# Performance work log

Hardware: AMD Instinct MI355X
Metric: run time of the kernel (lower is better)

The kernel has to match this reference:

```python
import jax, jax.numpy as jnp
import numpy as np

T, B, I, H = 512, 64, 1024, 1024
SIGMA = 0.01

def setup_inputs() -> dict:
    key = jax.random.key(0)
    k1, k2, k3 = jax.random.split(key, 3)
    X = jax.random.normal(k1, (T, B, I), dtype=jnp.float32)
    W_xh = jax.random.normal(k2, (I, H), dtype=jnp.float32) * SIGMA
    W_hh = jax.random.normal(k3, (H, H), dtype=jnp.float32) * SIGMA
    b_h = jnp.zeros((H,), dtype=jnp.float32)
    return {"X": X, "W_xh": W_xh, "W_hh": W_hh, "b_h": b_h}

def reference(X, W_xh, W_hh, b_h):
    # Precompute input projection for all timesteps in one big GEMM: [T,B,I]@[I,H]
    Xp = jnp.einsum('tbi,ih->tbh', X, W_xh) + b_h
    state0 = jnp.zeros((X.shape[1], W_hh.shape[0]), dtype=X.dtype)

    def step(state, xp_t):
        new_state = jnp.tanh(xp_t + state @ W_hh)
        return new_state, new_state

    final_state, outputs = jax.lax.scan(step, state0, Xp)
    return outputs, final_state
```

## Files before the change

### kernel.cpp

```cpp
#include <hip/hip_runtime.h>
#include <hip/hip_bf16.h>
#include <stdint.h>

typedef short bf16x8 __attribute__((ext_vector_type(8)));
typedef float f32x4  __attribute__((ext_vector_type(4)));
typedef unsigned int u32x4 __attribute__((ext_vector_type(4)));
typedef unsigned int u32x2 __attribute__((ext_vector_type(2)));

static __device__ __forceinline__ unsigned short bf16_rne(float f) {
    unsigned u = __builtin_bit_cast(unsigned, f);
    unsigned r = u + 0x7fffu + ((u >> 16) & 1u);
    return (unsigned short)(r >> 16);
}
static __device__ __forceinline__ float bf16tof(unsigned short h) {
    unsigned u = ((unsigned)h) << 16;
    return __builtin_bit_cast(float, u);
}

__global__ __launch_bounds__(256) void k_transpose(const float* __restrict__ W,
                                                   unsigned short* __restrict__ Wt) {
    __shared__ float tile[64][65];
    int bx = blockIdx.x & 15, by = blockIdx.x >> 4;
    int n0 = bx * 64, k0 = by * 64;
    int tx = threadIdx.x & 63, ty = threadIdx.x >> 6;
#pragma unroll
    for (int p = 0; p < 16; ++p) {
        int r = p * 4 + ty;
        tile[r][tx] = W[(size_t)(k0 + r) * 1024 + n0 + tx];
    }
    __syncthreads();
#pragma unroll
    for (int p = 0; p < 16; ++p) {
        int r = p * 4 + ty;
        Wt[(size_t)(n0 + r) * 1024 + k0 + tx] = bf16_rne(tile[tx][r]);
    }
}

#define LDA 80

__global__ __launch_bounds__(256) void k_xpgemm(const float* __restrict__ X,
                                                const unsigned short* __restrict__ Wt,
                                                const float* __restrict__ bh,
                                                unsigned short* __restrict__ Xp) {
    __shared__ __align__(16) unsigned char ldsA[128 * LDA];
    __shared__ __align__(16) unsigned char ldsB[128 * LDA];
    int p = blockIdx.x;
    int lo = (p & 7) * 256 + (p >> 3);
    int mt = lo >> 3, nt = lo & 7;
    int m0 = mt * 128, n0 = nt * 128;
    int tid = threadIdx.x;
    int lane = tid & 63, wid = tid >> 6;
    int wr = wid >> 1, wc = wid & 1;
    int mw = wr * 64, nw = wc * 64;
    int l15 = lane & 15, kg = lane >> 4;

    f32x4 acc[4][4] = {};
    int arow = tid >> 3, as = tid & 7;
    int brow = tid >> 2, bs = tid & 3;

    for (int kt = 0; kt < 32; ++kt) {
#pragma unroll
        for (int pp = 0; pp < 4; ++pp) {
            int r = pp * 32 + arow;
            const float4 v = *(const float4*)(X + (size_t)(m0 + r) * 1024 + kt * 32 + as * 4);
            unsigned lo32 = ((unsigned)bf16_rne(v.y) << 16) | bf16_rne(v.x);
            unsigned hi32 = ((unsigned)bf16_rne(v.w) << 16) | bf16_rne(v.z);
            *(uint2*)(ldsA + r * LDA + as * 8) = make_uint2(lo32, hi32);
        }
#pragma unroll
        for (int pp = 0; pp < 2; ++pp) {
            int r = pp * 64 + brow;
            uint4 v = *(const uint4*)(Wt + (size_t)(n0 + r) * 1024 + kt * 32 + bs * 8);
            *(uint4*)(ldsB + r * LDA + bs * 16) = v;
        }
        __syncthreads();
        bf16x8 af[4];
#pragma unroll
        for (int i = 0; i < 4; ++i)
            af[i] = *(const bf16x8*)(ldsA + (mw + 16 * i + l15) * LDA + kg * 16);
#pragma unroll
        for (int j = 0; j < 4; ++j) {
            bf16x8 bfj = *(const bf16x8*)(ldsB + (nw + 16 * j + l15) * LDA + kg * 16);
#pragma unroll
            for (int i = 0; i < 4; ++i)
                acc[i][j] = __builtin_amdgcn_mfma_f32_16x16x32_bf16(af[i], bfj, acc[i][j], 0, 0, 0);
        }
        __syncthreads();
    }
#pragma unroll
    for (int j = 0; j < 4; ++j) {
        int col = n0 + nw + 16 * j + l15;
        float bias = bh[col];
#pragma unroll
        for (int i = 0; i < 4; ++i) {
            int rb = m0 + mw + 16 * i + kg * 4;
#pragma unroll
            for (int r = 0; r < 4; ++r)
                Xp[(size_t)(rb + r) * 1024 + col] = bf16_rne(acc[i][j][r] + bias);
        }
    }
}

#define SB0 __builtin_amdgcn_sched_barrier(0)
#define WV0 asm volatile("s_waitcnt vmcnt(0)" ::: "memory")

template<int S> static __device__ __forceinline__ void ld16s(u32x4& d, uint64_t a) {
    if constexpr (S) asm volatile("global_load_dwordx4 %0, %1, off sc0" : "=v"(d) : "v"(a) : "memory");
    else             asm volatile("global_load_dwordx4 %0, %1, off sc1" : "=v"(d) : "v"(a) : "memory");
}
template<int S> static __device__ __forceinline__ void st8s(uint64_t a, u32x2 v) {
    if constexpr (S) asm volatile("global_store_dwordx2 %0, %1, off sc0" :: "v"(a), "v"(v) : "memory");
    else             asm volatile("global_store_dwordx2 %0, %1, off sc1" :: "v"(a), "v"(v) : "memory");
}
template<int S> static __device__ __forceinline__ void stds(uint64_t a, unsigned v) {
    if constexpr (S) asm volatile("global_store_dword %0, %1, off sc0" :: "v"(a), "v"(v) : "memory");
    else             asm volatile("global_store_dword %0, %1, off sc1" :: "v"(a), "v"(v) : "memory");
}
template<int S> static __device__ __forceinline__ unsigned lddw_wait(uint64_t a) {
    unsigned f;
    if constexpr (S) asm volatile("global_load_dword %0, %1, off sc0\n\ts_waitcnt vmcnt(0)" : "=v"(f) : "v"(a) : "memory");
    else             asm volatile("global_load_dword %0, %1, off sc1\n\ts_waitcnt vmcnt(0)" : "=v"(f) : "v"(a) : "memory");
    return f;
}
static __device__ __forceinline__ void st_sys(uint64_t a, unsigned v) {
    asm volatile("global_store_dword %0, %1, off sc0 sc1" :: "v"(a), "v"(v) : "memory");
}
static __device__ __forceinline__ unsigned ld_sys_wait(uint64_t a) {
    unsigned f;
    asm volatile("global_load_dword %0, %1, off sc0 sc1\n\ts_waitcnt vmcnt(0)" : "=v"(f) : "v"(a) : "memory");
    return f;
}

template<int S>
static __device__ __forceinline__ void scan_main(
    const float* __restrict__ Whh, const unsigned short* __restrict__ Xp,
    unsigned short* __restrict__ hbuf, unsigned* __restrict__ flags,
    float* __restrict__ out, unsigned char* lds, int chain, int mypos, int tid) {

    const int lane = tid & 63, wid = tid >> 6;
    const int l15 = lane & 15, kg = lane >> 4;
    const int jt = mypos * 128 + wid * 16;
    const int b  = chain * 16 + l15;
    const int jl = jt + kg * 4;

    bf16x8 w[32];
#pragma unroll
    for (int i = 0; i < 32; ++i)
#pragma unroll
        for (int e = 0; e < 8; ++e)
            w[i][e] = (short)bf16_rne(Whh[(size_t)(i * 32 + kg * 8 + e) * 1024 + jt + l15]);

    const uint64_t hb_c = (uint64_t)hbuf + (uint64_t)chain * 65536;
    const uint64_t fl_c = (uint64_t)flags + (uint64_t)chain * 64;
    const uint64_t fpoll = fl_c + (uint64_t)wid * 4;
    const uint64_t myflag = fl_c + (uint64_t)mypos * 4;

    const uint64_t crd = hb_c + (uint64_t)(lane >> 2) * 2048 + wid * 256 + (lane & 3) * 64;
    unsigned char* ldsw = lds + (lane >> 2) * 2064 + wid * 256 + (lane & 3) * 64;
    const unsigned char* lrd = lds + l15 * 2064 + kg * 16;

    const uint64_t hwr  = hb_c + (uint64_t)l15 * 2048 + (uint64_t)jl * 2;
    const uint64_t xpb  = (uint64_t)Xp + ((uint64_t)b * 1024 + jl) * 2;
    const uint64_t outb = (uint64_t)out + ((uint64_t)b * 1024 + jl) * 4;

    u32x2 xr;
    asm volatile("global_load_dwordx2 %0, %1, off" : "=v"(xr) : "v"(xpb) : "memory");

    f32x4 hv = {0.f, 0.f, 0.f, 0.f};

    for (int t = 0; t < 512; ++t) {
        if (t > 0) {
            unsigned tt = (unsigned)t;
            for (;;) { unsigned f = lddw_wait<S>(fpoll); if (__all(f >= tt)) break; }
        }
        u32x4 c0, c1, c2, c3;
        const uint64_t ca = crd + (uint64_t)(t & 1) * 32768;
        ld16s<S>(c0, ca); ld16s<S>(c1, ca + 16); ld16s<S>(c2, ca + 32); ld16s<S>(c3, ca + 48);
        WV0; SB0;
        *(u32x4*)(ldsw)      = c0; *(u32x4*)(ldsw + 16) = c1;
        *(u32x4*)(ldsw + 32) = c2; *(u32x4*)(ldsw + 48) = c3;
        __syncthreads();

        f32x4 a0 = {0.f, 0.f, 0.f, 0.f}, a1 = {0.f, 0.f, 0.f, 0.f};
        f32x4 a2 = {0.f, 0.f, 0.f, 0.f}, a3 = {0.f, 0.f, 0.f, 0.f};
#pragma unroll
        for (int ks = 0; ks < 8; ++ks) {
            a0 = __builtin_amdgcn_mfma_f32_16x16x32_bf16(
                w[4 * ks + 0], *(const bf16x8*)(lrd + (4 * ks + 0) * 64), a0, 0, 0, 0);
            a1 = __builtin_amdgcn_mfma_f32_16x16x32_bf16(
                w[4 * ks + 1], *(const bf16x8*)(lrd + (4 * ks + 1) * 64), a1, 0, 0, 0);
            a2 = __builtin_amdgcn_mfma_f32_16x16x32_bf16(
                w[4 * ks + 2], *(const bf16x8*)(lrd + (4 * ks + 2) * 64), a2, 0, 0, 0);
            a3 = __builtin_amdgcn_mfma_f32_16x16x32_bf16(
                w[4 * ks + 3], *(const bf16x8*)(lrd + (4 * ks + 3) * 64), a3, 0, 0, 0);
        }
        f32x4 acc = (a0 + a1) + (a2 + a3);

        float xpf[4] = { bf16tof((unsigned short)(xr[0] & 0xffffu)),
                         bf16tof((unsigned short)(xr[0] >> 16)),
                         bf16tof((unsigned short)(xr[1] & 0xffffu)),
                         bf16tof((unsigned short)(xr[1] >> 16)) };
        unsigned hb16[4];
#pragma unroll
        for (int r = 0; r < 4; ++r) {
            float z = acc[r] + xpf[r];
            z = fminf(fmaxf(z, -15.f), 15.f);
            float e = __expf(2.f * z);
            float v = (e - 1.f) / (e + 1.f);
            hv[r] = v;
            hb16[r] = (unsigned)bf16_rne(v);
        }

        if (t < 511) {
            u32x2 hh = { hb16[0] | (hb16[1] << 16), hb16[2] | (hb16[3] << 16) };
            st8s<S>(hwr + (uint64_t)((t + 1) & 1) * 32768, hh);
            WV0;
        }
        __syncthreads();
        if (t < 511 && tid == 0) stds<S>(myflag, (unsigned)(t + 1));

        if (t < 511)
            asm volatile("global_load_dwordx2 %0, %1, off"
                         : "=v"(xr) : "v"(xpb + (uint64_t)(t + 1) * 131072) : "memory");
        asm volatile("global_store_dwordx4 %0, %1, off"
                     :: "v"(outb + (uint64_t)t * 262144), "v"(hv) : "memory");
    }
    asm volatile("global_store_dwordx4 %0, %1, off"
                 :: "v"((uint64_t)out + ((uint64_t)33554432 + (uint64_t)b * 1024 + jl) * 4),
                    "v"(hv) : "memory");
}

__global__ __launch_bounds__(512) void k_scan(const float* __restrict__ Whh,
                                              const unsigned short* __restrict__ Xp,
                                              unsigned short* __restrict__ hbuf,
                                              unsigned int* flags,
                                              unsigned int* aux,
                                              float* __restrict__ out) {
    __shared__ __align__(16) unsigned char lds[16 * 2064];
    const int wgid = blockIdx.x, tid = threadIdx.x;
    const int lane = tid & 63, wid = tid >> 6;
    const int c8 = wgid & 7;
    if (c8 >= 4) return;
    const int chain = c8, mypos = wgid >> 3;
    const int windex = mypos * 4 + chain;
    const uint64_t A = (uint64_t)aux;
    const uint64_t F = (uint64_t)flags;

    unsigned xcc;
    asm volatile("s_getreg_b32 %0, hwreg(20, 0, 32)" : "=s"(xcc));
    xcc &= 7u;
    if (tid == 0) {
        if (mypos == 0) {
            uint64_t tm;
            asm volatile("s_memtime %0" : "=s"(tm));
            st_sys(F + 960 + (uint64_t)chain * 4, ((unsigned)tm ^ (unsigned)(tm >> 32)) | 1u);
        }
        st_sys(A + (uint64_t)windex * 4, xcc);
        WV0;
        st_sys(A + 128 + (uint64_t)windex * 4, 1u);
    }
    {
        uint64_t p = A + 128 + (uint64_t)(chain + 4 * (lane & 7)) * 4;
        for (;;) { unsigned f = ld_sys_wait(p); if (__all(f == 1u)) break; }
    }
    unsigned mapok;
    {
        unsigned x = ld_sys_wait(A + (uint64_t)(chain + 4 * (lane & 7)) * 4);
        unsigned x0 = (unsigned)__shfl((int)x, 0);
        mapok = __all(x == x0) ? 1u : 0u;
    }
    const unsigned nonce = ld_sys_wait(F + 960 + (uint64_t)chain * 4);

    const int l15 = lane & 15, kg = lane >> 4;
    const uint64_t hwr0 = (uint64_t)hbuf + (uint64_t)chain * 65536 +
                          (uint64_t)l15 * 2048 +
                          (uint64_t)(mypos * 128 + wid * 16 + kg * 4) * 2;
    if (mapok) {
#pragma unroll
        for (int par = 0; par < 2; ++par) {
            stds<1>(hwr0 + (uint64_t)par * 32768, 0u);
            stds<1>(hwr0 + (uint64_t)par * 32768 + 4, 0u);
        }
        if (tid == 0) {
            stds<1>(F + (uint64_t)chain * 64 + (uint64_t)mypos * 4, 0u);
            stds<1>(A + 640 + (uint64_t)windex * 4, 0u);
        }
        WV0;
    }
    __syncthreads();
    if (tid == 0) st_sys(A + 256 + (uint64_t)windex * 4, 1u);
    {
        uint64_t p = A + 256 + (uint64_t)(chain + 4 * (lane & 7)) * 4;
        for (;;) { unsigned f = ld_sys_wait(p); if (__all(f == 1u)) break; }
    }

    unsigned localok = mapok;
    if (mapok) {
        if (tid == 0) stds<1>(A + 640 + (uint64_t)windex * 4, nonce ^ (unsigned)windex);
        uint64_t p = A + 640 + (uint64_t)(chain + 4 * (lane & 7)) * 4;
        unsigned expv = nonce ^ (unsigned)(chain + 4 * (lane & 7));
        int ok = 0;
        for (int it = 0; it < 5000; ++it) {
            unsigned f = lddw_wait<1>(p);
            if (__all(f == expv)) { ok = 1; break; }
        }
        localok = (unsigned)ok;
    }
    if (tid == 0) {
        st_sys(A + 384 + (uint64_t)windex * 4, localok ? 1u : 2u);
        WV0;
        st_sys(A + 512 + (uint64_t)windex * 4, 1u);
    }
    {
        uint64_t p = A + 512 + (uint64_t)(chain + 4 * (lane & 7)) * 4;
        for (;;) { unsigned f = ld_sys_wait(p); if (__all(f == 1u)) break; }
    }
    unsigned v = ld_sys_wait(A + 384 + (uint64_t)(chain + 4 * (lane & 7)) * 4);
    const int FAST = __all(v == 1u) ? 1 : 0;
    __syncthreads();

    if (FAST) scan_main<1>(Whh, Xp, hbuf, flags, out, lds, chain, mypos, tid);
    else      scan_main<0>(Whh, Xp, hbuf, flags, out, lds, chain, mypos, tid);
}

extern "C" void kernel_launch(void* const* d_in, const int* in_sizes, int n_in,
                              void* d_out, int out_size, void* d_ws, size_t ws_size,
                              hipStream_t stream) {
    const float* X   = (const float*)d_in[0];
    const float* Wxh = (const float*)d_in[1];
    const float* Whh = (const float*)d_in[2];
    const float* bh  = (const float*)d_in[3];
    float* out = (float*)d_out;
    unsigned char* ws = (unsigned char*)d_ws;

    unsigned short* Wt    = (unsigned short*)(ws);
    unsigned short* Xp    = (unsigned short*)(ws + 2097152);
    unsigned short* hbuf  = (unsigned short*)(ws + 69206016);
    unsigned int*   flags = (unsigned int*)(ws + 69468160);
    unsigned int*   aux   = (unsigned int*)(ws + 69468416);

    hipMemsetAsync(ws + 69206016, 0, 263168, stream);
    hipLaunchKernelGGL(k_transpose, dim3(256), dim3(256), 0, stream, Wxh, Wt);
    hipLaunchKernelGGL(k_xpgemm, dim3(2048), dim3(256), 0, stream, X, Wt, bh, Xp);
    hipLaunchKernelGGL(k_scan, dim3(64), dim3(512), 0, stream, Whh, Xp, hbuf, flags, aux, out);
}
```

Before: 2.099 ms.

## Add a dedicated I/O wavefront to stage Xp loads and output stores via LDS

Each scan workgroup grows from 8 to 9 waves. The extra wave prefetches the Xp slices two steps ahead into double-buffered LDS and writes the previous step's hidden outputs from LDS to global memory. This takes the per-step Xp load and output store off the latency-critical recurrence waves. The cost is an extra barrier per step, coordinated with a double barrier in the I/O wave, more LDS use, and a larger block.

```diff
diff --git a/kernel.cpp b/kernel.cpp
--- a/kernel.cpp
+++ b/kernel.cpp
@@ -103,6 +103,10 @@
 
 #define SB0 __builtin_amdgcn_sched_barrier(0)
 #define WV0 asm volatile("s_waitcnt vmcnt(0)" ::: "memory")
+#define WLG0 asm volatile("s_waitcnt lgkmcnt(0)" ::: "memory")
+#define BAR do { asm volatile("" ::: "memory"); __builtin_amdgcn_sched_barrier(0); \
+                 __builtin_amdgcn_s_barrier(); \
+                 __builtin_amdgcn_sched_barrier(0); asm volatile("" ::: "memory"); } while (0)
 
 template<int S> static __device__ __forceinline__ void ld16s(u32x4& d, uint64_t a) {
     if constexpr (S) asm volatile("global_load_dwordx4 %0, %1, off sc0" : "=v"(d) : "v"(a) : "memory");
@@ -130,6 +134,12 @@
     asm volatile("global_load_dword %0, %1, off sc0 sc1\n\ts_waitcnt vmcnt(0)" : "=v"(f) : "v"(a) : "memory");
     return f;
 }
+#define LDX8(d, a) asm volatile("global_load_dwordx2 %0, %1, off" : "=v"(d) : "v"(a) : "memory")
+#define STOUT4(a, v) asm volatile("global_store_dwordx4 %0, %1, off" :: "v"(a), "v"(v) : "memory")
+
+#define L_SLICE 0
+#define L_OUT   33024
+#define L_XP    49408
 
 template<int S>
 static __device__ __forceinline__ void scan_main(
@@ -138,105 +148,146 @@
     float* __restrict__ out, unsigned char* lds, int chain, int mypos, int tid) {
 
     const int lane = tid & 63, wid = tid >> 6;
-    const int l15 = lane & 15, kg = lane >> 4;
-    const int jt = mypos * 128 + wid * 16;
-    const int b  = chain * 16 + l15;
-    const int jl = jt + kg * 4;
-
-    bf16x8 w[32];
-#pragma unroll
-    for (int i = 0; i < 32; ++i)
-#pragma unroll
-        for (int e = 0; e < 8; ++e)
-            w[i][e] = (short)bf16_rne(Whh[(size_t)(i * 32 + kg * 8 + e) * 1024 + jt + l15]);
-
     const uint64_t hb_c = (uint64_t)hbuf + (uint64_t)chain * 65536;
     const uint64_t fl_c = (uint64_t)flags + (uint64_t)chain * 64;
-    const uint64_t fpoll = fl_c + (uint64_t)wid * 4;
-    const uint64_t myflag = fl_c + (uint64_t)mypos * 4;
-
-    const uint64_t crd = hb_c + (uint64_t)(lane >> 2) * 2048 + wid * 256 + (lane & 3) * 64;
-    unsigned char* ldsw = lds + (lane >> 2) * 2064 + wid * 256 + (lane & 3) * 64;
-    const unsigned char* lrd = lds + l15 * 2064 + kg * 16;
-
-    const uint64_t hwr  = hb_c + (uint64_t)l15 * 2048 + (uint64_t)jl * 2;
-    const uint64_t xpb  = (uint64_t)Xp + ((uint64_t)b * 1024 + jl) * 2;
-    const uint64_t outb = (uint64_t)out + ((uint64_t)b * 1024 + jl) * 4;
-
-    u32x2 xr;
-    asm volatile("global_load_dwordx2 %0, %1, off" : "=v"(xr) : "v"(xpb) : "memory");
-
-    f32x4 hv = {0.f, 0.f, 0.f, 0.f};
-
-    for (int t = 0; t < 512; ++t) {
-        if (t > 0) {
-            unsigned tt = (unsigned)t;
-            for (;;) { unsigned f = lddw_wait<S>(fpoll); if (__all(f >= tt)) break; }
-        }
-        u32x4 c0, c1, c2, c3;
-        const uint64_t ca = crd + (uint64_t)(t & 1) * 32768;
-        ld16s<S>(c0, ca); ld16s<S>(c1, ca + 16); ld16s<S>(c2, ca + 32); ld16s<S>(c3, ca + 48);
-        WV0; SB0;
-        *(u32x4*)(ldsw)      = c0; *(u32x4*)(ldsw + 16) = c1;
-        *(u32x4*)(ldsw + 32) = c2; *(u32x4*)(ldsw + 48) = c3;
-        __syncthreads();
-
-        f32x4 a0 = {0.f, 0.f, 0.f, 0.f}, a1 = {0.f, 0.f, 0.f, 0.f};
-        f32x4 a2 = {0.f, 0.f, 0.f, 0.f}, a3 = {0.f, 0.f, 0.f, 0.f};
-#pragma unroll
-        for (int ks = 0; ks < 8; ++ks) {
-            a0 = __builtin_amdgcn_mfma_f32_16x16x32_bf16(
-                w[4 * ks + 0], *(const bf16x8*)(lrd + (4 * ks + 0) * 64), a0, 0, 0, 0);
-            a1 = __builtin_amdgcn_mfma_f32_16x16x32_bf16(
-                w[4 * ks + 1], *(const bf16x8*)(lrd + (4 * ks + 1) * 64), a1, 0, 0, 0);
-            a2 = __builtin_amdgcn_mfma_f32_16x16x32_bf16(
-                w[4 * ks + 2], *(const bf16x8*)(lrd + (4 * ks + 2) * 64), a2, 0, 0, 0);
-            a3 = __builtin_amdgcn_mfma_f32_16x16x32_bf16(
-                w[4 * ks + 3], *(const bf16x8*)(lrd + (4 * ks + 3) * 64), a3, 0, 0, 0);
-        }
-        f32x4 acc = (a0 + a1) + (a2 + a3);
-
-        float xpf[4] = { bf16tof((unsigned short)(xr[0] & 0xffffu)),
-                         bf16tof((unsigned short)(xr[0] >> 16)),
-                         bf16tof((unsigned short)(xr[1] & 0xffffu)),
-                         bf16tof((unsigned short)(xr[1] >> 16)) };
-        unsigned hb16[4];
-#pragma unroll
-        for (int r = 0; r < 4; ++r) {
-            float z = acc[r] + xpf[r];
-            z = fminf(fmaxf(z, -15.f), 15.f);
-            float e = __expf(2.f * z);
-            float v = (e - 1.f) / (e + 1.f);
-            hv[r] = v;
-            hb16[r] = (unsigned)bf16_rne(v);
-        }
-
-        if (t < 511) {
-            u32x2 hh = { hb16[0] | (hb16[1] << 16), hb16[2] | (hb16[3] << 16) };
-            st8s<S>(hwr + (uint64_t)((t + 1) & 1) * 32768, hh);
+
+    if (wid < 8) {
+        const int l15 = lane & 15, kg = lane >> 4;
+        const int jt = mypos * 128 + wid * 16;
+        const int b  = chain * 16 + l15;
+        const int jl = jt + kg * 4;
+
+        bf16x8 w[32];
+#pragma unroll
+        for (int i = 0; i < 32; ++i)
+#pragma unroll
+            for (int e = 0; e < 8; ++e)
+                w[i][e] = (short)bf16_rne(Whh[(size_t)(i * 32 + kg * 8 + e) * 1024 + jt + l15]);
+
+        const uint64_t fpoll = fl_c + (uint64_t)wid * 4;
+        const uint64_t myflag = fl_c + (uint64_t)mypos * 4;
+        const uint64_t crd = hb_c + (uint64_t)(lane >> 2) * 2048 + wid * 256 + (lane & 3) * 64;
+        unsigned char* ldsw = lds + L_SLICE + (lane >> 2) * 2064 + wid * 256 + (lane & 3) * 64;
+        const unsigned char* lrd = lds + L_SLICE + l15 * 2064 + kg * 16;
+        const uint64_t hwr = hb_c + (uint64_t)l15 * 2048 + (uint64_t)jl * 2;
+
+        f32x4 hv = {0.f, 0.f, 0.f, 0.f};
+
+        for (int t = 0; t < 512; ++t) {
+            if (t > 0) {
+                unsigned tt = (unsigned)t;
+                for (;;) { unsigned f = lddw_wait<S>(fpoll); if (__all(f >= tt)) break; }
+            }
+            BAR;
+            u32x4 c0, c1, c2, c3;
+            const uint64_t ca = crd + (uint64_t)(t & 1) * 32768;
+            ld16s<S>(c0, ca); ld16s<S>(c1, ca + 16); ld16s<S>(c2, ca + 32); ld16s<S>(c3, ca + 48);
+            WV0; SB0;
+            *(u32x4*)(ldsw)      = c0; *(u32x4*)(ldsw + 16) = c1;
+            *(u32x4*)(ldsw + 32) = c2; *(u32x4*)(ldsw + 48) = c3;
+            WLG0;
+            BAR;
+            f32x4 a0 = {0.f, 0.f, 0.f, 0.f}, a1 = {0.f, 0.f, 0.f, 0.f};
+            f32x4 a2 = {0.f, 0.f, 0.f, 0.f}, a3 = {0.f, 0.f, 0.f, 0.f};
+#pragma unroll
+            for (int ks = 0; ks < 8; ++ks) {
+                a0 = __builtin_amdgcn_mfma_f32_16x16x32_bf16(
+                    w[4 * ks + 0], *(const bf16x8*)(lrd + (4 * ks + 0) * 64), a0, 0, 0, 0);
+                a1 = __builtin_amdgcn_mfma_f32_16x16x32_bf16(
+                    w[4 * ks + 1], *(const bf16x8*)(lrd + (4 * ks + 1) * 64), a1, 0, 0, 0);
+                a2 = __builtin_amdgcn_mfma_f32_16x16x32_bf16(
+                    w[4 * ks + 2], *(const bf16x8*)(lrd + (4 * ks + 2) * 64), a2, 0, 0, 0);
+                a3 = __builtin_amdgcn_mfma_f32_16x16x32_bf16(
+                    w[4 * ks + 3], *(const bf16x8*)(lrd + (4 * ks + 3) * 64), a3, 0, 0, 0);
+            }
+            f32x4 acc = (a0 + a1) + (a2 + a3);
+
+            u32x2 xr = *(const u32x2*)(lds + L_XP + (t & 1) * 4096 + tid * 8);
+            float xpf[4] = { bf16tof((unsigned short)(xr[0] & 0xffffu)),
+                             bf16tof((unsigned short)(xr[0] >> 16)),
+                             bf16tof((unsigned short)(xr[1] & 0xffffu)),
+                             bf16tof((unsigned short)(xr[1] >> 16)) };
+            unsigned hb16[4];
+#pragma unroll
+            for (int r = 0; r < 4; ++r) {
+                float z = acc[r] + xpf[r];
+                z = fminf(fmaxf(z, -15.f), 15.f);
+                float e = __expf(2.f * z);
+                float v = (e - 1.f) / (e + 1.f);
+                hv[r] = v;
+                hb16[r] = (unsigned)bf16_rne(v);
+            }
+            *(f32x4*)(lds + L_OUT + (t & 1) * 8192 + tid * 16) = hv;
+            if (t < 511) {
+                u32x2 hh = { hb16[0] | (hb16[1] << 16), hb16[2] | (hb16[3] << 16) };
+                st8s<S>(hwr + (uint64_t)((t + 1) & 1) * 32768, hh);
+                WV0;
+            }
+            WLG0;
+            BAR;
+            if (t < 511 && tid == 0) stds<S>(myflag, (unsigned)(t + 1));
+        }
+        *(f32x4*)((float*)out + (size_t)33554432 + (size_t)b * 1024 + jl) = hv;
+    } else {
+        const int L = lane;
+        uint64_t xpb[8], outa[8];
+#pragma unroll
+        for (int ww = 0; ww < 8; ++ww) {
+            int bb = chain * 16 + (L & 15);
+            int col = mypos * 128 + ww * 16 + (L >> 4) * 4;
+            xpb[ww]  = (uint64_t)Xp + ((uint64_t)bb * 1024 + col) * 2;
+            outa[ww] = (uint64_t)out + ((uint64_t)bb * 1024 + col) * 4;
+        }
+        u32x2 xq[8];
+#pragma unroll
+        for (int ww = 0; ww < 8; ++ww) LDX8(xq[ww], xpb[ww]);
+        WV0;
+#pragma unroll
+        for (int ww = 0; ww < 8; ++ww)
+            *(u32x2*)(lds + L_XP + 0 * 4096 + (L + 64 * ww) * 8) = xq[ww];
+#pragma unroll
+        for (int ww = 0; ww < 8; ++ww) LDX8(xq[ww], xpb[ww] + 131072);
+        WLG0;
+
+        for (int t = 0; t < 512; ++t) {
+            BAR;
             WV0;
-        }
-        __syncthreads();
-        if (t < 511 && tid == 0) stds<S>(myflag, (unsigned)(t + 1));
-
-        if (t < 511)
-            asm volatile("global_load_dwordx2 %0, %1, off"
-                         : "=v"(xr) : "v"(xpb + (uint64_t)(t + 1) * 131072) : "memory");
-        asm volatile("global_store_dwordx4 %0, %1, off"
-                     :: "v"(outb + (uint64_t)t * 262144), "v"(hv) : "memory");
-    }
-    asm volatile("global_store_dwordx4 %0, %1, off"
-                 :: "v"((uint64_t)out + ((uint64_t)33554432 + (uint64_t)b * 1024 + jl) * 4),
-                    "v"(hv) : "memory");
-}
-
-__global__ __launch_bounds__(512) void k_scan(const float* __restrict__ Whh,
+            if (t < 511) {
+#pragma unroll
+                for (int ww = 0; ww < 8; ++ww)
+                    *(u32x2*)(lds + L_XP + ((t + 1) & 1) * 4096 + (L + 64 * ww) * 8) = xq[ww];
+            }
+            if (t > 0) {
+#pragma unroll
+                for (int ww = 0; ww < 8; ++ww) {
+                    u32x4 ov = *(const u32x4*)(lds + L_OUT + ((t - 1) & 1) * 8192 + (L + 64 * ww) * 16);
+                    STOUT4(outa[ww] + (uint64_t)(t - 1) * 262144, ov);
+                }
+            }
+            if (t < 510) {
+#pragma unroll
+                for (int ww = 0; ww < 8; ++ww)
+                    LDX8(xq[ww], xpb[ww] + (uint64_t)(t + 2) * 131072);
+            }
+            WLG0;
+            BAR;
+            BAR;
+        }
+#pragma unroll
+        for (int ww = 0; ww < 8; ++ww) {
+            u32x4 ov = *(const u32x4*)(lds + L_OUT + (511 & 1) * 8192 + (L + 64 * ww) * 16);
+            STOUT4(outa[ww] + (uint64_t)511 * 262144, ov);
+        }
+    }
+}
+
+__global__ __launch_bounds__(576) void k_scan(const float* __restrict__ Whh,
                                               const unsigned short* __restrict__ Xp,
                                               unsigned short* __restrict__ hbuf,
                                               unsigned int* flags,
                                               unsigned int* aux,
                                               float* __restrict__ out) {
-    __shared__ __align__(16) unsigned char lds[16 * 2064];
+    __shared__ __align__(16) unsigned char lds[57600];
     const int wgid = blockIdx.x, tid = threadIdx.x;
     const int lane = tid & 63, wid = tid >> 6;
     const int c8 = wgid & 7;
@@ -271,11 +322,11 @@
     }
     const unsigned nonce = ld_sys_wait(F + 960 + (uint64_t)chain * 4);
 
-    const int l15 = lane & 15, kg = lane >> 4;
+    const int l15 = lane & 15;
     const uint64_t hwr0 = (uint64_t)hbuf + (uint64_t)chain * 65536 +
                           (uint64_t)l15 * 2048 +
-                          (uint64_t)(mypos * 128 + wid * 16 + kg * 4) * 2;
-    if (mapok) {
+                          (uint64_t)(mypos * 128 + wid * 16 + (lane >> 4) * 4) * 2;
+    if (mapok && wid < 8) {
 #pragma unroll
         for (int par = 0; par < 2; ++par) {
             stds<1>(hwr0 + (uint64_t)par * 32768, 0u);
@@ -342,5 +393,5 @@
     hipMemsetAsync(ws + 69206016, 0, 263168, stream);
     hipLaunchKernelGGL(k_transpose, dim3(256), dim3(256), 0, stream, Wxh, Wt);
     hipLaunchKernelGGL(k_xpgemm, dim3(2048), dim3(256), 0, stream, X, Wt, bh, Xp);
-    hipLaunchKernelGGL(k_scan, dim3(64), dim3(512), 0, stream, Whh, Xp, hbuf, flags, aux, out);
-}
+    hipLaunchKernelGGL(k_scan, dim3(64), dim3(576), 0, stream, Whh, Xp, hbuf, flags, aux, out);
+}
```

Result: no change. 2.139 ms (+1.9%).
